# Kernel tuning notes

Hardware: AMD Instinct MI355X
Metric: run time of the kernel (lower is better)

Reference implementation:

```python
import jax, jax.numpy as jnp
import numpy as np

EPS = 1e-12


def _complex_log(x):
    # log of a real tensor as a complex number: log|x| + i*pi*[x<0]
    real = jnp.log(jnp.maximum(jnp.abs(x), EPS))
    imag = jnp.where(x < 0, jnp.pi, 0.0).astype(jnp.float32)
    return jax.lax.complex(real.astype(jnp.float32), imag)


def _logcumsumexp_complex(x, axis):
    # numerically-stable complex logcumsumexp via associative scan
    def logaddexp_c(a, b):
        m = jnp.maximum(a.real, b.real)  # real-valued max for stability
        return jnp.log(jnp.exp(a - m) + jnp.exp(b - m)) + m
    return jax.lax.associative_scan(logaddexp_c, x, axis=axis)


def setup_inputs() -> dict:
    key = jax.random.key(0)
    ks = jax.random.split(key, 7)
    b, d, l, n = 2, 1024, 1024, 16
    u = jax.random.normal(ks[0], (b, d, l), dtype=jnp.float32)
    delta = jax.random.normal(ks[1], (b, d, l), dtype=jnp.float32)
    # A negative (like Mamba's A = -exp(A_log)) so the scan stays stable
    A = -(0.5 + jax.random.uniform(ks[2], (d, n), dtype=jnp.float32))
    B = jax.random.normal(ks[3], (b, n, l), dtype=jnp.float32)
    C = jax.random.normal(ks[4], (b, n, l), dtype=jnp.float32)
    D = jax.random.normal(ks[5], (d,), dtype=jnp.float32)
    z = jax.random.normal(ks[6], (b, d, l), dtype=jnp.float32)
    return {"u": u, "delta": delta, "A": A, "B": B, "C": C, "D": D, "z": z}


def reference(u, delta, A, B, C, D, z):
    # delta_softplus=True path of SelectiveScanTorch.forward
    dt = jax.nn.softplus(delta)                                   # (b,d,l)
    dA = jnp.einsum('bdl,dn->bldn', dt, A)                        # (b,l,d,n)
    dB_u = jnp.einsum('bdl,bdl,bnl->bldn', dt, u, B)              # (b,l,d,n)

    dB_u_log = _complex_log(dB_u)                                 # complex64
    # dA_star[l] = sum_{k=1}^{l} dA[k]  (exclusive of step 0, front-padded)
    dA_star = jnp.pad(jnp.cumsum(dA[:, 1:], axis=1),
                      ((0, 0), (1, 0), (0, 0), (0, 0)))
    x_log = _logcumsumexp_complex(dB_u_log - dA_star, axis=1) + dA_star

    x_real = jnp.exp(x_log.real) * jnp.cos(x_log.imag)            # (b,l,d,n)
    y = jnp.einsum('bldn,bnl->bdl', x_real.astype(C.dtype), C)    # (b,d,l)
    out = y + u * D[None, :, None]
    return (out * jax.nn.silu(z)).astype(u.dtype)
```

## Files before the change

kernel.cpp:

```cpp
#include <hip/hip_runtime.h>
#include <math.h>

namespace {

constexpr int kD = 1024;
constexpr int kL = 1024;
constexpr int kN = 16;
constexpr int kE = 8;
constexpr int kJ = 8;
constexpr int kT = 256;

__global__ __launch_bounds__(kT)
void selscan(const float* __restrict__ u,
             const float* __restrict__ delta,
             const float* __restrict__ A,
             const float* __restrict__ Bm,
             const float* __restrict__ Cm,
             const float* __restrict__ Dv,
             const float* __restrict__ z,
             float* __restrict__ out)
{
    __shared__ float2 sax[128][kN + 1];
    __shared__ float2 sw[4][kN];

    const int bd   = blockIdx.x;
    const int b    = bd >> 10;
    const int d    = bd & (kD - 1);
    const int t    = threadIdx.x;
    const int lane = t & 63;
    const int wave = t >> 6;
    const int nh   = t & 1;
    const int n0   = nh << 3;
    const int chunk = t >> 1;
    const int l0   = chunk << 3;
    const size_t base = (size_t)bd * kL;

    const float LOG2E = 1.4426950408889634f;
    const float LN2   = 0.6931471805599453f;

    float dt[kE], dtu[kE];
    {
        float4 d0 = *(const float4*)(delta + base + l0);
        float4 d1 = *(const float4*)(delta + base + l0 + 4);
        float4 u0 = *(const float4*)(u + base + l0);
        float4 u1 = *(const float4*)(u + base + l0 + 4);
        float dd[kE] = {d0.x,d0.y,d0.z,d0.w,d1.x,d1.y,d1.z,d1.w};
        float uu[kE] = {u0.x,u0.y,u0.z,u0.w,u1.x,u1.y,u1.z,u1.w};
        #pragma unroll
        for (int s = 0; s < kE; ++s) {
            float x = dd[s];
            float e = __builtin_amdgcn_exp2f(-fabsf(x) * LOG2E);
            float sp = fmaxf(x, 0.f) + __builtin_amdgcn_logf(1.f + e) * LN2;
            dt[s]  = sp;
            dtu[s] = sp * uu[s];
        }
    }

    float cj[kJ];
    {
        float4 a0 = *(const float4*)(A + d * kN + n0);
        float4 a1 = *(const float4*)(A + d * kN + n0 + 4);
        cj[0]=a0.x*LOG2E; cj[1]=a0.y*LOG2E; cj[2]=a0.z*LOG2E; cj[3]=a0.w*LOG2E;
        cj[4]=a1.x*LOG2E; cj[5]=a1.y*LOG2E; cj[6]=a1.z*LOG2E; cj[7]=a1.w*LOG2E;
    }

    float Q[kJ][kE];
    float y[kE] = {0.f,0.f,0.f,0.f,0.f,0.f,0.f,0.f};
    const int rowbase = (b << 4) + n0;
    #pragma unroll
    for (int j = 0; j < kJ; ++j) {
        const float* Bp = Bm + (size_t)(rowbase + j) * kL + l0;
        const float* Cp = Cm + (size_t)(rowbase + j) * kL + l0;
        float4 b0 = *(const float4*)Bp;
        float4 b1 = *(const float4*)(Bp + 4);
        float4 c0 = *(const float4*)Cp;
        float4 c1 = *(const float4*)(Cp + 4);
        float Bv[kE] = {b0.x,b0.y,b0.z,b0.w,b1.x,b1.y,b1.z,b1.w};
        float Cv[kE] = {c0.x,c0.y,c0.z,c0.w,c1.x,c1.y,c1.z,c1.w};
        float x = 0.f, p = 1.f;
        #pragma unroll
        for (int s = 0; s < kE; ++s) {
            float e = __builtin_amdgcn_exp2f(dt[s] * cj[j]);
            x = fmaf(e, x, dtu[s] * Bv[s]);
            p *= e;
            Q[j][s] = p * Cv[s];
            y[s] = fmaf(x, Cv[s], y[s]);
        }
        sax[chunk][n0 + j] = make_float2(p, x);
    }
    __syncthreads();

    {
        const int sn = lane & 15;
        const int q  = lane >> 4;
        const int cb = (wave << 5) + (q << 3);

        float p = 1.f, c = 0.f;
        #pragma unroll
        for (int i = 0; i < 8; ++i) {
            float2 ax = sax[cb + i][sn];
            c = fmaf(ax.x, c, ax.y);
            p *= ax.x;
        }
        float Aq = p, Xq = c;
        {
            float ain = __shfl_up(Aq, 16, 64);
            float xin = __shfl_up(Xq, 16, 64);
            bool act = (lane >= 16);
            Xq = fmaf(Aq, act ? xin : 0.f, Xq);
            Aq *= act ? ain : 1.f;
            ain = __shfl_up(Aq, 32, 64);
            xin = __shfl_up(Xq, 32, 64);
            act = (lane >= 32);
            Xq = fmaf(Aq, act ? xin : 0.f, Xq);
            Aq *= act ? ain : 1.f;
        }
        if (q == 3) sw[wave][sn] = make_float2(Aq, Xq);
        float eA = __shfl_up(Aq, 16, 64);
        float eX = __shfl_up(Xq, 16, 64);
        if (lane < 16) { eA = 1.f; eX = 0.f; }
        __syncthreads();
        float wx = 0.f;
        if (wave > 0) {
            wx = sw[0][sn].y;
            if (wave > 1) { float2 s1 = sw[1][sn]; wx = fmaf(s1.x, wx, s1.y); }
            if (wave > 2) { float2 s2 = sw[2][sn]; wx = fmaf(s2.x, wx, s2.y); }
        }
        float cc = fmaf(eA, wx, eX);
        #pragma unroll
        for (int i = 0; i < 8; ++i) {
            float2 ax = sax[cb + i][sn];
            sax[cb + i][sn].x = cc;
            cc = fmaf(ax.x, cc, ax.y);
        }
    }
    __syncthreads();

    #pragma unroll
    for (int j = 0; j < kJ; ++j) {
        float carry = sax[chunk][n0 + j].x;
        #pragma unroll
        for (int s = 0; s < kE; ++s)
            y[s] = fmaf(carry, Q[j][s], y[s]);
    }

    #pragma unroll
    for (int s = 0; s < kE; ++s) y[s] += __shfl_xor(y[s], 1, 64);

    const float D_d = Dv[d];
    float y0, y1, y2, y3;
    if (nh == 0) { y0 = y[0]; y1 = y[1]; y2 = y[2]; y3 = y[3]; }
    else         { y0 = y[4]; y1 = y[5]; y2 = y[6]; y3 = y[7]; }

    const int eoff = l0 + nh * 4;
    float4 zv = *(const float4*)(z + base + eoff);
    float4 uv = *(const float4*)(u + base + eoff);
    float s0 = __builtin_amdgcn_rcpf(1.f + __builtin_amdgcn_exp2f(-zv.x * LOG2E));
    float s1 = __builtin_amdgcn_rcpf(1.f + __builtin_amdgcn_exp2f(-zv.y * LOG2E));
    float s2 = __builtin_amdgcn_rcpf(1.f + __builtin_amdgcn_exp2f(-zv.z * LOG2E));
    float s3 = __builtin_amdgcn_rcpf(1.f + __builtin_amdgcn_exp2f(-zv.w * LOG2E));
    float4 o;
    o.x = (y0 + uv.x * D_d) * zv.x * s0;
    o.y = (y1 + uv.y * D_d) * zv.y * s1;
    o.z = (y2 + uv.z * D_d) * zv.z * s2;
    o.w = (y3 + uv.w * D_d) * zv.w * s3;
    *(float4*)(out + base + eoff) = o;
}

}

extern "C" void kernel_launch(void* const* d_in, const int* in_sizes, int n_in,
                              void* d_out, int out_size, void* d_ws, size_t ws_size,
                              hipStream_t stream) {
    const float* u     = (const float*)d_in[0];
    const float* delta = (const float*)d_in[1];
    const float* A     = (const float*)d_in[2];
    const float* Bm    = (const float*)d_in[3];
    const float* Cm    = (const float*)d_in[4];
    const float* Dv    = (const float*)d_in[5];
    const float* z     = (const float*)d_in[6];
    float* out = (float*)d_out;

    dim3 grid(2 * kD);
    dim3 block(kT);
    hipLaunchKernelGGL(selscan, grid, block, 0, stream,
                       u, delta, A, Bm, Cm, Dv, z, out);
}
```

Before: 27.51 us.

## Split state halves across waves, halve per-thread chunk, double block size

Moves to 512 threads per block, each handling 4 timesteps instead of 8. The two halves of the state dimension now go to separate wave groups rather than adjacent lanes. The shared scan buffer is transposed to [n][chunk], the cross-wave prefix is extended to 8 waves, and the y partial sums are combined through shared memory with an extra barrier instead of a lane shuffle. A and D are now scalarised with readfirstlane. The goal is more parallelism and lower per-thread register pressure, at the cost of an extra sync and having half the threads idle during the epilogue.

```diff
diff --git a/kernel.cpp b/kernel.cpp
--- a/kernel.cpp
+++ b/kernel.cpp
@@ -6,9 +6,15 @@
 constexpr int kD = 1024;
 constexpr int kL = 1024;
 constexpr int kN = 16;
-constexpr int kE = 8;
+constexpr int kE = 4;
 constexpr int kJ = 8;
-constexpr int kT = 256;
+constexpr int kT = 512;
+constexpr int kC = 256;
+constexpr int kCP = kC + 1;
+
+__device__ __forceinline__ float rfl(float x) {
+    return __uint_as_float(__builtin_amdgcn_readfirstlane(__float_as_uint(x)));
+}
 
 __global__ __launch_bounds__(kT)
 void selscan(const float* __restrict__ u,
@@ -20,8 +26,9 @@
              const float* __restrict__ z,
              float* __restrict__ out)
 {
-    __shared__ float2 sax[128][kN + 1];
-    __shared__ float2 sw[4][kN];
+    __shared__ float2 sax[kN][kCP];
+    __shared__ float2 sw[8][kN];
+    __shared__ float2 syr[kC][3];
 
     const int bd   = blockIdx.x;
     const int b    = bd >> 10;
@@ -29,64 +36,59 @@
     const int t    = threadIdx.x;
     const int lane = t & 63;
     const int wave = t >> 6;
-    const int nh   = t & 1;
+    const int nh   = wave >> 2;
     const int n0   = nh << 3;
-    const int chunk = t >> 1;
-    const int l0   = chunk << 3;
+    const int chunk = ((wave & 3) << 6) | lane;
+    const int l0   = chunk << 2;
     const size_t base = (size_t)bd * kL;
 
     const float LOG2E = 1.4426950408889634f;
     const float LN2   = 0.6931471805599453f;
 
-    float dt[kE], dtu[kE];
+    float dt2[kE], dtu[kE];
     {
-        float4 d0 = *(const float4*)(delta + base + l0);
-        float4 d1 = *(const float4*)(delta + base + l0 + 4);
-        float4 u0 = *(const float4*)(u + base + l0);
-        float4 u1 = *(const float4*)(u + base + l0 + 4);
-        float dd[kE] = {d0.x,d0.y,d0.z,d0.w,d1.x,d1.y,d1.z,d1.w};
-        float uu[kE] = {u0.x,u0.y,u0.z,u0.w,u1.x,u1.y,u1.z,u1.w};
+        float4 dv = *(const float4*)(delta + base + l0);
+        float4 uv = *(const float4*)(u + base + l0);
+        float dd[4] = {dv.x, dv.y, dv.z, dv.w};
+        float uu[4] = {uv.x, uv.y, uv.z, uv.w};
         #pragma unroll
         for (int s = 0; s < kE; ++s) {
             float x = dd[s];
             float e = __builtin_amdgcn_exp2f(-fabsf(x) * LOG2E);
             float sp = fmaxf(x, 0.f) + __builtin_amdgcn_logf(1.f + e) * LN2;
-            dt[s]  = sp;
+            dt2[s] = sp * LOG2E;
             dtu[s] = sp * uu[s];
         }
     }
 
-    float cj[kJ];
+    float aj[kJ];
     {
-        float4 a0 = *(const float4*)(A + d * kN + n0);
-        float4 a1 = *(const float4*)(A + d * kN + n0 + 4);
-        cj[0]=a0.x*LOG2E; cj[1]=a0.y*LOG2E; cj[2]=a0.z*LOG2E; cj[3]=a0.w*LOG2E;
-        cj[4]=a1.x*LOG2E; cj[5]=a1.y*LOG2E; cj[6]=a1.z*LOG2E; cj[7]=a1.w*LOG2E;
+        const float* Ap = A + d * kN + n0;
+        #pragma unroll
+        for (int j = 0; j < kJ; ++j) aj[j] = rfl(Ap[j]);
     }
 
     float Q[kJ][kE];
-    float y[kE] = {0.f,0.f,0.f,0.f,0.f,0.f,0.f,0.f};
+    float y[kE] = {0.f, 0.f, 0.f, 0.f};
     const int rowbase = (b << 4) + n0;
     #pragma unroll
     for (int j = 0; j < kJ; ++j) {
         const float* Bp = Bm + (size_t)(rowbase + j) * kL + l0;
         const float* Cp = Cm + (size_t)(rowbase + j) * kL + l0;
-        float4 b0 = *(const float4*)Bp;
-        float4 b1 = *(const float4*)(Bp + 4);
-        float4 c0 = *(const float4*)Cp;
-        float4 c1 = *(const float4*)(Cp + 4);
-        float Bv[kE] = {b0.x,b0.y,b0.z,b0.w,b1.x,b1.y,b1.z,b1.w};
-        float Cv[kE] = {c0.x,c0.y,c0.z,c0.w,c1.x,c1.y,c1.z,c1.w};
+        float4 b4 = *(const float4*)Bp;
+        float4 c4 = *(const float4*)Cp;
+        float Bv[4] = {b4.x, b4.y, b4.z, b4.w};
+        float Cv[4] = {c4.x, c4.y, c4.z, c4.w};
         float x = 0.f, p = 1.f;
         #pragma unroll
         for (int s = 0; s < kE; ++s) {
-            float e = __builtin_amdgcn_exp2f(dt[s] * cj[j]);
+            float e = __builtin_amdgcn_exp2f(dt2[s] * aj[j]);
             x = fmaf(e, x, dtu[s] * Bv[s]);
             p *= e;
             Q[j][s] = p * Cv[s];
             y[s] = fmaf(x, Cv[s], y[s]);
         }
-        sax[chunk][n0 + j] = make_float2(p, x);
+        sax[n0 + j][chunk] = make_float2(p, x);
     }
     __syncthreads();
 
@@ -98,7 +100,7 @@
         float p = 1.f, c = 0.f;
         #pragma unroll
         for (int i = 0; i < 8; ++i) {
-            float2 ax = sax[cb + i][sn];
+            float2 ax = sax[sn][cb + i];
             c = fmaf(ax.x, c, ax.y);
             p *= ax.x;
         }
@@ -120,17 +122,20 @@
         float eX = __shfl_up(Xq, 16, 64);
         if (lane < 16) { eA = 1.f; eX = 0.f; }
         __syncthreads();
+
         float wx = 0.f;
-        if (wave > 0) {
-            wx = sw[0][sn].y;
-            if (wave > 1) { float2 s1 = sw[1][sn]; wx = fmaf(s1.x, wx, s1.y); }
-            if (wave > 2) { float2 s2 = sw[2][sn]; wx = fmaf(s2.x, wx, s2.y); }
+        #pragma unroll
+        for (int w = 0; w < 7; ++w) {
+            if (w < wave) {
+                float2 s2 = sw[w][sn];
+                wx = fmaf(s2.x, wx, s2.y);
+            }
         }
         float cc = fmaf(eA, wx, eX);
         #pragma unroll
         for (int i = 0; i < 8; ++i) {
-            float2 ax = sax[cb + i][sn];
-            sax[cb + i][sn].x = cc;
+            float2 ax = sax[sn][cb + i];
+            sax[sn][cb + i].x = cc;
             cc = fmaf(ax.x, cc, ax.y);
         }
     }
@@ -138,33 +143,40 @@
 
     #pragma unroll
     for (int j = 0; j < kJ; ++j) {
-        float carry = sax[chunk][n0 + j].x;
+        float carry = sax[n0 + j][chunk].x;
         #pragma unroll
         for (int s = 0; s < kE; ++s)
             y[s] = fmaf(carry, Q[j][s], y[s]);
     }
 
-    #pragma unroll
-    for (int s = 0; s < kE; ++s) y[s] += __shfl_xor(y[s], 1, 64);
-
-    const float D_d = Dv[d];
-    float y0, y1, y2, y3;
-    if (nh == 0) { y0 = y[0]; y1 = y[1]; y2 = y[2]; y3 = y[3]; }
-    else         { y0 = y[4]; y1 = y[5]; y2 = y[6]; y3 = y[7]; }
-
-    const int eoff = l0 + nh * 4;
-    float4 zv = *(const float4*)(z + base + eoff);
-    float4 uv = *(const float4*)(u + base + eoff);
-    float s0 = __builtin_amdgcn_rcpf(1.f + __builtin_amdgcn_exp2f(-zv.x * LOG2E));
-    float s1 = __builtin_amdgcn_rcpf(1.f + __builtin_amdgcn_exp2f(-zv.y * LOG2E));
-    float s2 = __builtin_amdgcn_rcpf(1.f + __builtin_amdgcn_exp2f(-zv.z * LOG2E));
-    float s3 = __builtin_amdgcn_rcpf(1.f + __builtin_amdgcn_exp2f(-zv.w * LOG2E));
-    float4 o;
-    o.x = (y0 + uv.x * D_d) * zv.x * s0;
-    o.y = (y1 + uv.y * D_d) * zv.y * s1;
-    o.z = (y2 + uv.z * D_d) * zv.z * s2;
-    o.w = (y3 + uv.w * D_d) * zv.w * s3;
-    *(float4*)(out + base + eoff) = o;
+    if (nh == 1) {
+        syr[chunk][0] = make_float2(y[0], y[1]);
+        syr[chunk][1] = make_float2(y[2], y[3]);
+    }
+    __syncthreads();
+
+    if (nh == 0) {
+        float2 ya = syr[chunk][0];
+        float2 yb = syr[chunk][1];
+        float y0 = y[0] + ya.x;
+        float y1 = y[1] + ya.y;
+        float y2 = y[2] + yb.x;
+        float y3 = y[3] + yb.y;
+
+        const float D_d = rfl(Dv[d]);
+        float4 uv = *(const float4*)(u + base + l0);
+        float4 zv = *(const float4*)(z + base + l0);
+        float s0 = __builtin_amdgcn_rcpf(1.f + __builtin_amdgcn_exp2f(-zv.x * LOG2E));
+        float s1 = __builtin_amdgcn_rcpf(1.f + __builtin_amdgcn_exp2f(-zv.y * LOG2E));
+        float s2 = __builtin_amdgcn_rcpf(1.f + __builtin_amdgcn_exp2f(-zv.z * LOG2E));
+        float s3 = __builtin_amdgcn_rcpf(1.f + __builtin_amdgcn_exp2f(-zv.w * LOG2E));
+        float4 o;
+        o.x = (y0 + uv.x * D_d) * zv.x * s0;
+        o.y = (y1 + uv.y * D_d) * zv.y * s1;
+        o.z = (y2 + uv.z * D_d) * zv.z * s2;
+        o.w = (y3 + uv.w * D_d) * zv.w * s3;
+        *(float4*)(out + base + l0) = o;
+    }
 }
 
 }
```

Result: faster. 22.01 us (median of 3 runs) (-20.0%).
